# Kernel optimization log

Measured on AMD Instinct MI355X. Metric: run time of the kernel, lower is better.

Reference implementation:

```python
import math
import jax, jax.numpy as jnp
import numpy as np

EPS_LN = 1e-5
EPS_NORM = 1e-12


def conv2d(x, w, b=None, groups=1):
    # x: (B,C,H,W), w: (O, I//groups, kh, kw)
    out = jax.lax.conv_general_dilated(
        x, w, window_strides=(1, 1), padding='SAME',
        dimension_numbers=('NCHW', 'OIHW', 'NCHW'),
        feature_group_count=groups)
    if b is not None:
        out = out + b[None, :, None, None]
    return out


def layernorm2d(x, w, b):
    # LayerNorm over channel dim of (B,C,H,W)
    mu = x.mean(axis=1, keepdims=True)
    var = ((x - mu) ** 2).mean(axis=1, keepdims=True)
    xn = (x - mu) / jnp.sqrt(var + EPS_LN)
    return xn * w[None, :, None, None] + b[None, :, None, None]


def l2norm(x):
    n = jnp.sqrt((x * x).sum(axis=-1, keepdims=True))
    return x / jnp.maximum(n, EPS_NORM)


def mha(s, Wi, bi, Wo, bo, num_heads):
    # torch nn.MultiheadAttention (batch_first) self-attention
    B, S, C = s.shape
    Dh = C // num_heads
    qkv = s @ Wi.T + bi                      # (B,S,3C)
    q, k, v = jnp.split(qkv, 3, axis=-1)
    hd = lambda t: t.reshape(B, S, num_heads, Dh).transpose(0, 2, 1, 3)
    q, k, v = hd(q), hd(k), hd(v)            # (B,H,S,Dh)
    attn = jax.nn.softmax(jnp.einsum('bhqd,bhkd->bhqk', q, k) / math.sqrt(Dh), axis=-1)
    o = jnp.einsum('bhqk,bhkd->bhqd', attn, v).transpose(0, 2, 1, 3).reshape(B, S, C)
    return o @ Wo.T + bo


def frfn(x, pconv_w, lin1_w, lin1_b, dw_w, dw_b, lin2_w, lin2_b):
    b, c, h, w = x.shape
    dc = c // 4
    x1 = conv2d(x[:, :dc], pconv_w)                       # partial conv, no bias
    x = jnp.concatenate([x1, x[:, dc:]], axis=1)
    xt = x.transpose(0, 2, 3, 1).reshape(b, h * w, c)
    y = jax.nn.gelu(xt @ lin1_w.T + lin1_b, approximate=False)  # (b,hw,2*hid)
    y1, y2 = jnp.split(y, 2, axis=-1)
    hid = lin1_w.shape[0] // 2
    y1 = y1.reshape(b, h, w, hid).transpose(0, 3, 1, 2)
    y1 = jax.nn.gelu(conv2d(y1, dw_w, dw_b, groups=hid), approximate=False)
    y1 = y1.transpose(0, 2, 3, 1).reshape(b, h * w, hid)
    out = (y1 * y2) @ lin2_w.T + lin2_b
    return out.reshape(b, h, w, c).transpose(0, 3, 1, 2)


def setup_inputs() -> dict:
    key = jax.random.key(0)
    ks = jax.random.split(key, 10)
    B, C, H, W = 16, 256, 64, 64
    HID = 2 * C  # FRFN hidden = embed_dim*2
    DC = C // 4
    w = lambda k, shape: (jax.random.normal(k, shape, dtype=jnp.float32) * 0.02)
    return {
        'x': jax.random.normal(ks[0], (B, C, H, W), dtype=jnp.float32),
        'slot_scale': jnp.asarray(C ** -0.5, dtype=jnp.float32),
        'norm1_w': jnp.ones((C,), jnp.float32), 'norm1_b': jnp.zeros((C,), jnp.float32),
        'in_proj_w': w(ks[1], (3 * C, C)), 'in_proj_b': jnp.zeros((3 * C,), jnp.float32),
        'out_proj_w': w(ks[2], (C, C)), 'out_proj_b': jnp.zeros((C,), jnp.float32),
        'norm2_w': jnp.ones((C,), jnp.float32), 'norm2_b': jnp.zeros((C,), jnp.float32),
        'pconv_w': w(ks[3], (DC, DC, 3, 3)),
        'lin1_w': w(ks[4], (2 * HID, C)), 'lin1_b': jnp.zeros((2 * HID,), jnp.float32),
        'dw_w': w(ks[5], (HID, 1, 3, 3)), 'dw_b': jnp.zeros((HID,), jnp.float32),
        'lin2_w': w(ks[6], (C, HID)), 'lin2_b': jnp.zeros((C,), jnp.float32),
    }


def reference(x, slot_scale, norm1_w, norm1_b, in_proj_w, in_proj_b,
              out_proj_w, out_proj_b, norm2_w, norm2_b,
              pconv_w, lin1_w, lin1_b, dw_w, dw_b, lin2_w, lin2_b):
    NUM_HEADS, POOL = 8, 8
    b, c, h, w = x.shape
    copy = x
    # ada_avgpool slot init: 8x8 exact block means (h,w divisible by pool)
    pooled = x.reshape(b, c, POOL, h // POOL, POOL, w // POOL).mean(axis=(3, 5))  # (b,c,8,8)
    init_slots = pooled.transpose(0, 2, 3, 1).reshape(b, POOL * POOL, c)          # (b,S,c)

    shortcut = x
    xn = layernorm2d(x, norm1_w, norm1_b)
    xf = xn.transpose(0, 2, 3, 1).reshape(b, h * w, c)                            # (b,N,c)
    logits = slot_scale * jnp.einsum('bsc,bnc->bsn', l2norm(init_slots), l2norm(xf))
    slots = jnp.einsum('bsn,bnc->bsc', jax.nn.softmax(logits, axis=-1), xf)
    slots = mha(slots, in_proj_w, in_proj_b, out_proj_w, out_proj_b, NUM_HEADS)
    out = jnp.einsum('bns,bsc->bnc', jax.nn.softmax(logits.transpose(0, 2, 1), axis=-1), slots)
    out = out.transpose(0, 2, 1).reshape(b, c, h, w)

    x = shortcut + out
    x = x + frfn(layernorm2d(x, norm2_w, norm2_b),
                 pconv_w, lin1_w, lin1_b, dw_w, dw_b, lin2_w, lin2_b)
    return (x, copy - x)
```

## Files before the change

### kernel.cpp

```cpp
#include <hip/hip_runtime.h>
#include <hip/hip_bf16.h>
#include <stdint.h>
#include <math.h>

#define BB 16
#define CC 256
#define HH 64
#define WW 64
#define NN 4096
#define SS 64
#define NHEAD 8
#define DH 32
#define HID 512
#define DC 64

typedef float    f32x4  __attribute__((ext_vector_type(4)));
typedef uint16_t u16x8  __attribute__((ext_vector_type(8)));
typedef uint16_t u16x4  __attribute__((ext_vector_type(4)));
typedef uint16_t u16x2  __attribute__((ext_vector_type(2)));

__device__ __forceinline__ float gelu_fast(float x){
  float u = 0.7978845608028654f * (x + 0.044715f * x * x * x);
  float e = __expf(2.0f * u);
  float th = 1.0f - 2.0f / (e + 1.0f);
  return 0.5f * x * (1.0f + th);
}
__device__ __forceinline__ uint16_t f2b(float f){
  union { float f; uint32_t u; } v; v.f = f;
  uint32_t r = v.u + 0x7fffu + ((v.u >> 16) & 1u);
  return (uint16_t)(r >> 16);
}
__device__ __forceinline__ float b2f(uint16_t h){
  union { uint32_t u; float f; } v; v.u = ((uint32_t)h) << 16;
  return v.f;
}

__device__ __forceinline__ float waveSum(float v){
#pragma unroll
  for (int m = 32; m >= 1; m >>= 1) v += __shfl_xor(v, m, 64);
  return v;
}
__device__ __forceinline__ float blockSum256(float v, float* s4){
  v = waveSum(v);
  __syncthreads();
  if ((threadIdx.x & 63) == 0) s4[threadIdx.x >> 6] = v;
  __syncthreads();
  return s4[0] + s4[1] + s4[2] + s4[3];
}

__device__ __forceinline__ void g2l16(const void* g, void* l){
  __builtin_amdgcn_global_load_lds((const __attribute__((address_space(1))) uint32_t*)g,
                                   (__attribute__((address_space(3))) uint32_t*)l, 16, 0, 0);
}

__device__ __forceinline__ int swz8(int row, int kp){ return (kp ^ (row & 7)) << 3; }

__device__ __forceinline__ void mfma_bf16(f32x4& d, u16x8 a, u16x8 b){
  asm volatile("v_mfma_f32_16x16x32_bf16 %0, %1, %2, %0" : "+v"(d) : "v"(a), "v"(b));
}

template<int SWA, int SWB>
__device__ __forceinline__ void mma_core(const uint16_t* lA, int lda, const uint16_t* lB, int ldb,
                                         f32x4 (&acc)[4][4], int wrow, int wcol, int lane){
  const int rb = lane & 15, ub = lane >> 4;
#pragma unroll
  for (int ks = 0; ks < 2; ks++){
    const int u = ks * 4 + ub;
    u16x8 af[4], bf[4];
#pragma unroll
    for (int m = 0; m < 4; m++){
      int r = wrow + m * 16 + rb;
      int e = SWA ? ((u ^ (r & 7)) << 3) : (u << 3);
      af[m] = *(const u16x8*)&lA[r * lda + e];
    }
#pragma unroll
    for (int n = 0; n < 4; n++){
      int r = wcol + n * 16 + rb;
      int e = SWB ? ((u ^ (r & 7)) << 3) : (u << 3);
      bf[n] = *(const u16x8*)&lB[r * ldb + e];
    }
#pragma unroll
    for (int m = 0; m < 4; m++)
#pragma unroll
      for (int n = 0; n < 4; n++)
        mfma_bf16(acc[m][n], af[m], bf[n]);
  }
}

__global__ __launch_bounds__(256) void k_t2b(const float* __restrict__ in, uint16_t* __restrict__ out){
  __shared__ float tile[64][33];
  int b = blockIdx.z;
  int n0 = blockIdx.x * 32;
  int c0 = blockIdx.y * 64;
  int tx = threadIdx.x, ty = threadIdx.y;
  const float* src = in + (size_t)b * CC * NN;
#pragma unroll
  for (int i = 0; i < 64; i += 8)
    tile[ty + i][tx] = src[(size_t)(c0 + ty + i) * NN + n0 + tx];
  __syncthreads();
  uint16_t* dst = out + (size_t)b * NN * CC;
#pragma unroll
  for (int i = 0; i < 32; i += 8){
    int r = ty + i;
    u16x2 o; o[0] = f2b(tile[tx * 2][r]); o[1] = f2b(tile[tx * 2 + 1][r]);
    *(u16x2*)&dst[(size_t)(n0 + r) * CC + c0 + tx * 2] = o;
  }
}

__global__ __launch_bounds__(256) void k_pool(const uint16_t* __restrict__ xhwcb, uint16_t* __restrict__ slotsNb){
  int bs = blockIdx.x; int b = bs >> 6, s = bs & 63;
  int sy = (s >> 3) * 8, sx = (s & 7) * 8;
  int t = threadIdx.x;
  int c4 = t & 63, pg = t >> 6;
  const uint16_t* base = xhwcb + (size_t)b * NN * CC;
  float a0 = 0.f, a1 = 0.f, a2 = 0.f, a3 = 0.f;
#pragma unroll
  for (int i = 0; i < 16; i++){
    int p = pg * 16 + i; int py = p >> 3, px = p & 7;
    u16x4 v = *(const u16x4*)&base[(size_t)((sy + py) * WW + sx + px) * CC + c4 * 4];
    a0 += b2f(v[0]); a1 += b2f(v[1]); a2 += b2f(v[2]); a3 += b2f(v[3]);
  }
  __shared__ float sm[4][64][4];
  sm[pg][c4][0] = a0; sm[pg][c4][1] = a1; sm[pg][c4][2] = a2; sm[pg][c4][3] = a3;
  __syncthreads();
  if (t < 64){
    float v0 = (sm[0][t][0] + sm[1][t][0] + sm[2][t][0] + sm[3][t][0]) * (1.0f / 64.0f);
    float v1 = (sm[0][t][1] + sm[1][t][1] + sm[2][t][1] + sm[3][t][1]) * (1.0f / 64.0f);
    float v2 = (sm[0][t][2] + sm[1][t][2] + sm[2][t][2] + sm[3][t][2]) * (1.0f / 64.0f);
    float v3 = (sm[0][t][3] + sm[1][t][3] + sm[2][t][3] + sm[3][t][3]) * (1.0f / 64.0f);
    float ss = waveSum(v0 * v0 + v1 * v1 + v2 * v2 + v3 * v3);
    float inv = 1.0f / fmaxf(sqrtf(ss), 1e-12f);
    u16x4 o; o[0] = f2b(v0 * inv); o[1] = f2b(v1 * inv); o[2] = f2b(v2 * inv); o[3] = f2b(v3 * inv);
    *(u16x4*)&slotsNb[(size_t)bs * CC + t * 4] = o;
  }
}

__global__ __launch_bounds__(256) void k_ln_w(const uint16_t* __restrict__ xa, const uint16_t* __restrict__ xb,
                                              const float* __restrict__ w, const float* __restrict__ b,
                                              uint16_t* __restrict__ xoutb, float* __restrict__ rn,
                                              uint16_t* __restrict__ xn2p){
  int row = blockIdx.x * 4 + (threadIdx.x >> 6);
  int lane = threadIdx.x & 63;
  u16x4 va = *(const u16x4*)&xa[(size_t)row * CC + lane * 4];
  float v0 = b2f(va[0]), v1 = b2f(va[1]), v2 = b2f(va[2]), v3 = b2f(va[3]);
  if (xb){
    u16x4 vb = *(const u16x4*)&xb[(size_t)row * CC + lane * 4];
    v0 += b2f(vb[0]); v1 += b2f(vb[1]); v2 += b2f(vb[2]); v3 += b2f(vb[3]);
  }
  float mu = waveSum(v0 + v1 + v2 + v3) * (1.0f / CC);
  float d0 = v0 - mu, d1 = v1 - mu, d2 = v2 - mu, d3 = v3 - mu;
  float var = waveSum(d0 * d0 + d1 * d1 + d2 * d2 + d3 * d3) * (1.0f / CC);
  float inv = rsqrtf(var + 1e-5f);
  float4 wv = *(const float4*)&w[lane * 4];
  float4 bv = *(const float4*)&b[lane * 4];
  float x0 = d0 * inv * wv.x + bv.x;
  float x1 = d1 * inv * wv.y + bv.y;
  float x2 = d2 * inv * wv.z + bv.z;
  float x3 = d3 * inv * wv.w + bv.w;
  u16x4 o; o[0] = f2b(x0); o[1] = f2b(x1); o[2] = f2b(x2); o[3] = f2b(x3);
  *(u16x4*)&xoutb[(size_t)row * CC + lane * 4] = o;
  if (xn2p && lane < 16){
    int bb = row >> 12, n = row & 4095, y = n >> 6, x = n & 63;
    *(u16x4*)&xn2p[(((size_t)(bb * 66 + y + 1)) * 66 + x + 1) * 64 + lane * 4] = o;
  }
  if (rn){
    float ss = waveSum(x0 * x0 + x1 * x1 + x2 * x2 + x3 * x3);
    if (lane == 0) rn[row] = 1.0f / fmaxf(sqrtf(ss), 1e-12f);
  }
}

__global__ __launch_bounds__(256) void k_zb(uint16_t* __restrict__ xn2p){
  int i = blockIdx.x * 256 + threadIdx.x;
  if (i >= 16 * 260 * 16) return;
  int c4 = i & 15; int rest = i >> 4;
  int j = rest % 260; int b = rest / 260;
  int py, px;
  if (j < 66){ py = 0; px = j; }
  else if (j < 132){ py = 65; px = j - 66; }
  else if (j < 196){ py = j - 132 + 1; px = 0; }
  else { py = j - 196 + 1; px = 65; }
  u16x4 z; z[0] = 0; z[1] = 0; z[2] = 0; z[3] = 0;
  *(u16x4*)&xn2p[(((size_t)(b * 66 + py)) * 66 + px) * 64 + c4 * 4] = z;
}

__global__ __launch_bounds__(256) void k_cvtw(const float* __restrict__ wi, const float* __restrict__ wo,
                                              const float* __restrict__ w1, const float* __restrict__ w2,
                                              const float* __restrict__ pw, const float* __restrict__ dww,
                                              uint16_t* __restrict__ wib, uint16_t* __restrict__ wob,
                                              uint16_t* __restrict__ w1b, uint16_t* __restrict__ w2b,
                                              uint16_t* __restrict__ wp2, float* __restrict__ dwwT){
  int i = blockIdx.x * 256 + threadIdx.x;
  if (i < 163840){
    const float* src; uint16_t* dst; int off;
    if (i < 49152){ src = wi; dst = wib; off = i; }
    else if (i < 65536){ src = wo; dst = wob; off = i - 49152; }
    else if (i < 131072){ src = w1; dst = w1b; off = i - 65536; }
    else { src = w2; dst = w2b; off = i - 131072; }
    float4 v = ((const float4*)src)[off];
    u16x4 o;
    o[0] = f2b(v.x); o[1] = f2b(v.y); o[2] = f2b(v.z); o[3] = f2b(v.w);
    *(u16x4*)&dst[(size_t)off * 4] = o;
  } else if (i < 200704){
    int j = i - 163840;
    if (j < 64 * 576){
      int co = j / 576, r = j % 576, tap = r >> 6, ci = r & 63;
      wp2[j] = f2b(pw[(size_t)co * 576 + ci * 9 + tap]);
    }
  } else {
    int j = i - 200704;
    if (j < 9 * HID){
      int tap = j / HID, ch = j % HID;
      dwwT[j] = dww[(size_t)ch * 9 + tap];
    }
  }
}

__global__ __launch_bounds__(256) void k_logits_mfma(const uint16_t* __restrict__ slotsNb,
                                                     const uint16_t* __restrict__ xnb,
                                                     const float* __restrict__ rn,
                                                     const float* __restrict__ scale_p,
                                                     uint16_t* __restrict__ E){
  __shared__ uint16_t smem[20480];
  __shared__ float rnS[256];
  uint16_t* lA = smem;
  uint16_t* lB = smem + 64 * 64;
  int t = threadIdx.x, lane = t & 63, w = t >> 6;
  int b = blockIdx.y, n0 = blockIdx.x * 256;
  rnS[t] = rn[b * NN + n0 + t];
  f32x4 acc[4][4];
#pragma unroll
  for (int m = 0; m < 4; m++)
#pragma unroll
    for (int n = 0; n < 4; n++) acc[m][n] = (f32x4){0.f, 0.f, 0.f, 0.f};
  for (int kc = 0; kc < 4; kc++){
#pragma unroll
    for (int i = 0; i < 2; i++){
      int idx = i * 256 + t, row = idx >> 3, kp = idx & 7;
      *(u16x8*)&lA[row * 64 + swz8(row, kp)] = *(const u16x8*)&slotsNb[(size_t)(b * 64 + row) * 256 + kc * 64 + kp * 8];
    }
#pragma unroll
    for (int i = 0; i < 8; i++){
      int idx = i * 256 + t, row = idx >> 3, kp = idx & 7;
      *(u16x8*)&lB[row * 64 + swz8(row, kp)] = *(const u16x8*)&xnb[((size_t)b * NN + n0 + row) * 256 + kc * 64 + kp * 8];
    }
    __syncthreads();
    mma_core<1, 1>(lA, 64, lB, 64, acc, 0, w * 64, lane);
    __syncthreads();
  }
  float scale = scale_p[0];
  int rb4 = (lane >> 4) * 4, cb = lane & 15;
#pragma unroll
  for (int m = 0; m < 4; m++)
#pragma unroll
    for (int n = 0; n < 4; n++)
#pragma unroll
      for (int j = 0; j < 4; j++){
        int s = m * 16 + rb4 + j, nl = w * 64 + n * 16 + cb;
        smem[s * 264 + nl] = f2b(__expf(acc[m][n][j] * scale * rnS[nl]));
      }
  __syncthreads();
#pragma unroll
  for (int i = 0; i < 8; i++){
    int idx = i * 256 + t, row = idx >> 5, cseg = idx & 31;
    *(u16x8*)&E[((size_t)b * 64 + row) * NN + n0 + cseg * 8] = *(const u16x8*)&smem[row * 264 + cseg * 8];
  }
}

__global__ __launch_bounds__(256) void k_z1(const uint16_t* __restrict__ E, float* __restrict__ invz1){
  int bs = blockIdx.x, t = threadIdx.x;
  u16x8 v0 = *(const u16x8*)&E[(size_t)bs * NN + t * 16];
  u16x8 v1 = *(const u16x8*)&E[(size_t)bs * NN + t * 16 + 8];
  float s = 0.f;
#pragma unroll
  for (int i = 0; i < 8; i++) s += b2f(v0[i]) + b2f(v1[i]);
  __shared__ float s4[4];
  float z = blockSum256(s, s4);
  if (t == 0) invz1[bs] = 1.0f / z;
}

__global__ __launch_bounds__(256) void k_slots_mfma(const uint16_t* __restrict__ E,
                                                    const uint16_t* __restrict__ xnb,
                                                    float* __restrict__ part){
  __shared__ uint16_t lA[64 * 64];
  __shared__ uint16_t lB[256 * 72];
  int t = threadIdx.x, lane = t & 63, w = t >> 6;
  int ks = blockIdx.x, b = blockIdx.y;
  f32x4 acc[4][4];
#pragma unroll
  for (int m = 0; m < 4; m++)
#pragma unroll
    for (int n = 0; n < 4; n++) acc[m][n] = (f32x4){0.f, 0.f, 0.f, 0.f};
  for (int kc = 0; kc < 8; kc++){
    int n0 = ks * 512 + kc * 64;
#pragma unroll
    for (int i = 0; i < 2; i++){
      int idx = i * 256 + t, row = idx >> 3, kp = idx & 7;
      *(u16x8*)&lA[row * 64 + swz8(row, kp)] = *(const u16x8*)&E[((size_t)b * 64 + row) * NN + n0 + kp * 8];
    }
#pragma unroll
    for (int i = 0; i < 8; i++){
      int idx = i * 256 + t, nrow = idx >> 5, cseg = idx & 31;
      u16x8 v = *(const u16x8*)&xnb[((size_t)b * NN + n0 + nrow) * 256 + cseg * 8];
#pragma unroll
      for (int j = 0; j < 8; j++) lB[(cseg * 8 + j) * 72 + nrow] = v[j];
    }
    __syncthreads();
    mma_core<1, 0>(lA, 64, lB, 72, acc, 0, w * 64, lane);
    __syncthreads();
  }
  int rb4 = (lane >> 4) * 4, cb = lane & 15;
#pragma unroll
  for (int m = 0; m < 4; m++)
#pragma unroll
    for (int n = 0; n < 4; n++)
#pragma unroll
      for (int j = 0; j < 4; j++){
        int s = m * 16 + rb4 + j, c = w * 64 + n * 16 + cb;
        part[(((size_t)b * 8 + ks) * 64 + s) * 256 + c] = acc[m][n][j];
      }
}

__global__ __launch_bounds__(256) void k_fold(const float* __restrict__ part, const float* __restrict__ invz1,
                                              uint16_t* __restrict__ slotsb){
  int i = blockIdx.x * 256 + threadIdx.x;
  int row = i >> 6, c4 = i & 63;
  int b = row >> 6, s = row & 63;
  float4 a = {0.f, 0.f, 0.f, 0.f};
#pragma unroll
  for (int p = 0; p < 8; p++){
    float4 v = *(const float4*)&part[(((size_t)b * 8 + p) * 64 + s) * 256 + c4 * 4];
    a.x += v.x; a.y += v.y; a.z += v.z; a.w += v.w;
  }
  float iz = invz1[row];
  u16x4 o; o[0] = f2b(a.x * iz); o[1] = f2b(a.y * iz); o[2] = f2b(a.z * iz); o[3] = f2b(a.w * iz);
  *(u16x4*)&slotsb[(size_t)row * 256 + c4 * 4] = o;
}

__global__ __launch_bounds__(256) void k_gemm_qkv(const uint16_t* __restrict__ slotsb,
                                                  const uint16_t* __restrict__ wib,
                                                  const float* __restrict__ bi,
                                                  float* __restrict__ qkv){
  __shared__ uint16_t lA[128 * 64];
  __shared__ uint16_t lB[128 * 64];
  int t = threadIdx.x, lane = t & 63, w = t >> 6;
  int wrow = (w >> 1) * 64, wcol = (w & 1) * 64;
  int BR = blockIdx.x * 128, BC = blockIdx.y * 128;
  f32x4 acc[4][4];
#pragma unroll
  for (int m = 0; m < 4; m++)
#pragma unroll
    for (int n = 0; n < 4; n++) acc[m][n] = (f32x4){0.f, 0.f, 0.f, 0.f};
  for (int kc = 0; kc < 4; kc++){
#pragma unroll
    for (int i = 0; i < 4; i++){
      int idx = i * 256 + t, row = idx >> 3, kp = idx & 7;
      *(u16x8*)&lA[row * 64 + swz8(row, kp)] = *(const u16x8*)&slotsb[(size_t)(BR + row) * 256 + kc * 64 + kp * 8];
      *(u16x8*)&lB[row * 64 + swz8(row, kp)] = *(const u16x8*)&wib[(size_t)(BC + row) * 256 + kc * 64 + kp * 8];
    }
    __syncthreads();
    mma_core<1, 1>(lA, 64, lB, 64, acc, wrow, wcol, lane);
    __syncthreads();
  }
  int rb4 = (lane >> 4) * 4, cb = lane & 15;
#pragma unroll
  for (int m = 0; m < 4; m++)
#pragma unroll
    for (int n = 0; n < 4; n++){
      int c = BC + wcol + n * 16 + cb;
      float bias = bi[c];
#pragma unroll
      for (int j = 0; j < 4; j++)
        qkv[(size_t)(BR + wrow + m * 16 + rb4 + j) * 768 + c] = acc[m][n][j] + bias;
    }
}

__global__ __launch_bounds__(256) void k_attn(const float* __restrict__ qkv, uint16_t* __restrict__ aob){
  int b = blockIdx.x >> 3, h = blockIdx.x & 7;
  __shared__ float lq[64][33], lk[64][33], lv[64][33];
  __shared__ float sc[64][65];
  int t = threadIdx.x;
  for (int idx = t; idx < 64 * 32; idx += 256){
    int s = idx >> 5, d = idx & 31;
    const float* base = qkv + ((size_t)b * SS + s) * 768 + h * DH + d;
    lq[s][d] = base[0];
    lk[s][d] = base[256];
    lv[s][d] = base[512];
  }
  __syncthreads();
  const float rs = 0.17677669529663687f;
  for (int idx = t; idx < 64 * 64; idx += 256){
    int qq = idx >> 6, kk = idx & 63;
    float a = 0.f;
#pragma unroll
    for (int d = 0; d < 32; d++) a += lq[qq][d] * lk[kk][d];
    sc[qq][kk] = a * rs;
  }
  __syncthreads();
  {
    int r = t >> 2, sub = t & 3;
    float m = -1e30f;
#pragma unroll
    for (int k = sub * 16; k < sub * 16 + 16; k++) m = fmaxf(m, sc[r][k]);
    m = fmaxf(m, __shfl_xor(m, 1, 64));
    m = fmaxf(m, __shfl_xor(m, 2, 64));
    float z = 0.f;
#pragma unroll
    for (int k = sub * 16; k < sub * 16 + 16; k++){
      float e = __expf(sc[r][k] - m); sc[r][k] = e; z += e;
    }
    z += __shfl_xor(z, 1, 64);
    z += __shfl_xor(z, 2, 64);
    float iv = 1.0f / z;
#pragma unroll
    for (int k = sub * 16; k < sub * 16 + 16; k++) sc[r][k] *= iv;
  }
  __syncthreads();
  for (int idx = t; idx < 64 * 32; idx += 256){
    int qq = idx >> 5, d = idx & 31;
    float a = 0.f;
#pragma unroll
    for (int k = 0; k < 64; k++) a += sc[qq][k] * lv[k][d];
    aob[((size_t)b * SS + qq) * CC + h * DH + d] = f2b(a);
  }
}

__global__ __launch_bounds__(256) void k_gemm_oproj(const uint16_t* __restrict__ aob,
                                                    const uint16_t* __restrict__ wob,
                                                    const float* __restrict__ bo,
                                                    uint16_t* __restrict__ sl2Tb){
  __shared__ uint16_t lA[128 * 64];
  __shared__ uint16_t lB[128 * 64];
  int t = threadIdx.x, lane = t & 63, w = t >> 6;
  int wrow = (w >> 1) * 64, wcol = (w & 1) * 64;
  int BR = blockIdx.x * 128, BC = blockIdx.y * 128;
  f32x4 acc[4][4];
#pragma unroll
  for (int m = 0; m < 4; m++)
#pragma unroll
    for (int n = 0; n < 4; n++) acc[m][n] = (f32x4){0.f, 0.f, 0.f, 0.f};
  for (int kc = 0; kc < 4; kc++){
#pragma unroll
    for (int i = 0; i < 4; i++){
      int idx = i * 256 + t, row = idx >> 3, kp = idx & 7;
      *(u16x8*)&lA[row * 64 + swz8(row, kp)] = *(const u16x8*)&aob[(size_t)(BR + row) * 256 + kc * 64 + kp * 8];
      *(u16x8*)&lB[row * 64 + swz8(row, kp)] = *(const u16x8*)&wob[(size_t)(BC + row) * 256 + kc * 64 + kp * 8];
    }
    __syncthreads();
    mma_core<1, 1>(lA, 64, lB, 64, acc, wrow, wcol, lane);
    __syncthreads();
  }
  int rb4 = (lane >> 4) * 4, cb = lane & 15;
#pragma unroll
  for (int m = 0; m < 4; m++)
#pragma unroll
    for (int n = 0; n < 4; n++){
      int c = BC + wcol + n * 16 + cb;
      float bias = bo[c];
#pragma unroll
      for (int j = 0; j < 4; j++){
        int r = BR + wrow + m * 16 + rb4 + j;
        int b = r >> 6, s = r & 63;
        sl2Tb[((size_t)b * 256 + c) * 64 + s] = f2b(acc[m][n][j] + bias);
      }
    }
}

__global__ __launch_bounds__(256) void k_mix(const uint16_t* __restrict__ E, const uint16_t* __restrict__ sl2Tb,
                                             uint16_t* __restrict__ mixb){
  __shared__ uint16_t lA[128 * 72];
  __shared__ uint16_t lB[128 * 64];
  __shared__ float z2S[128];
  int t = threadIdx.x, lane = t & 63, w = t >> 6;
  int wrow = (w >> 1) * 64, wcol = (w & 1) * 64;
  int BR = blockIdx.x * 128, BC = blockIdx.y * 128, b = blockIdx.z;
#pragma unroll
  for (int i = 0; i < 4; i++){
    int idx = i * 256 + t; int s = idx >> 4, n8 = (idx & 15) * 8;
    u16x8 v = *(const u16x8*)&E[((size_t)b * 64 + s) * NN + BR + n8];
#pragma unroll
    for (int j = 0; j < 8; j++) lA[(n8 + j) * 72 + s] = v[j];
  }
#pragma unroll
  for (int i = 0; i < 4; i++){
    int idx = i * 256 + t, row = idx >> 3, kp = idx & 7;
    *(u16x8*)&lB[row * 64 + swz8(row, kp)] = *(const u16x8*)&sl2Tb[((size_t)b * 256 + BC + row) * 64 + kp * 8];
  }
  __syncthreads();
  if (t < 128){
    float s = 0.f;
#pragma unroll
    for (int k2 = 0; k2 < 64; k2++) s += b2f(lA[t * 72 + k2]);
    z2S[t] = 1.0f / s;
  }
  __syncthreads();
  f32x4 acc[4][4];
#pragma unroll
  for (int m = 0; m < 4; m++)
#pragma unroll
    for (int n = 0; n < 4; n++) acc[m][n] = (f32x4){0.f, 0.f, 0.f, 0.f};
  mma_core<0, 1>(lA, 72, lB, 64, acc, wrow, wcol, lane);
  int rb4 = (lane >> 4) * 4, cb = lane & 15;
#pragma unroll
  for (int m = 0; m < 4; m++)
#pragma unroll
    for (int n = 0; n < 4; n++)
#pragma unroll
      for (int j = 0; j < 4; j++){
        int lrow = wrow + m * 16 + rb4 + j;
        size_t gi = ((size_t)b * NN + BR + lrow) * 256 + BC + wcol + n * 16 + cb;
        mixb[gi] = f2b(acc[m][n][j] * z2S[lrow]);
      }
}

__global__ __launch_bounds__(256) void k_pconv_mfma(const uint16_t* __restrict__ xn2p,
                                                    const uint16_t* __restrict__ wp2,
                                                    uint16_t* __restrict__ pcb){
  __shared__ uint16_t lA[256 * 64];
  __shared__ uint16_t lB[64 * 64];
  int t = threadIdx.x, lane = t & 63, w = t >> 6;
  int wrow = w * 64;
  int BR = blockIdx.x * 256;
  f32x4 acc[4][4];
#pragma unroll
  for (int m = 0; m < 4; m++)
#pragma unroll
    for (int n = 0; n < 4; n++) acc[m][n] = (f32x4){0.f, 0.f, 0.f, 0.f};
  for (int tap = 0; tap < 9; tap++){
    int dy = tap / 3 - 1, dx = tap % 3 - 1;
#pragma unroll
    for (int i = 0; i < 8; i++){
      int q = (w * 8 + i) * 64 + lane;
      int row = q >> 3, kpe = swz8(row, q & 7);
      int r = BR + row;
      int b = r >> 12, n = r & 4095, y = n >> 6, x = n & 63;
      size_t p = ((size_t)(b * 66 + (y + 1 + dy)) * 66 + (x + 1 + dx)) * 64 + kpe;
      g2l16(&xn2p[p], &lA[(w * 8 + i) * 512]);
    }
#pragma unroll
    for (int i = 0; i < 2; i++){
      int q = (w * 2 + i) * 64 + lane;
      int row = q >> 3, kpe = swz8(row, q & 7);
      g2l16(&wp2[(size_t)row * 576 + tap * 64 + kpe], &lB[(w * 2 + i) * 512]);
    }
    __syncthreads();
    mma_core<1, 1>(lA, 64, lB, 64, acc, wrow, 0, lane);
    __syncthreads();
  }
  int rb4 = (lane >> 4) * 4, cb = lane & 15;
#pragma unroll
  for (int m = 0; m < 4; m++)
#pragma unroll
    for (int n = 0; n < 4; n++)
#pragma unroll
      for (int j = 0; j < 4; j++)
        pcb[(size_t)(BR + wrow + m * 16 + rb4 + j) * 64 + (n * 16 + cb)] = f2b(acc[m][n][j]);
}

__global__ __launch_bounds__(256) void k_lin1_mfma(const uint16_t* __restrict__ pcb,
                                                   const uint16_t* __restrict__ xn2b,
                                                   const uint16_t* __restrict__ w1b,
                                                   const float* __restrict__ b1,
                                                   uint16_t* __restrict__ Y1b, uint16_t* __restrict__ Y2b){
  __shared__ uint16_t lA[128 * 64];
  __shared__ uint16_t lB[128 * 64];
  int t = threadIdx.x, lane = t & 63, w = t >> 6;
  int wrow = (w >> 1) * 64, wcol = (w & 1) * 64;
  int bid = blockIdx.x;
  int xcd = bid & 7, i5 = bid >> 3;
  int BR = (xcd * 64 + (i5 >> 3)) * 128;
  int BC = (i5 & 7) * 128;
  f32x4 acc[4][4];
#pragma unroll
  for (int m = 0; m < 4; m++)
#pragma unroll
    for (int n = 0; n < 4; n++) acc[m][n] = (f32x4){0.f, 0.f, 0.f, 0.f};
  for (int kc = 0; kc < 4; kc++){
#pragma unroll
    for (int i = 0; i < 4; i++){
      int q = (w * 4 + i) * 64 + lane;
      int row = q >> 3, kpe = swz8(row, q & 7);
      size_t gr = (size_t)(BR + row);
      const uint16_t* src = (kc == 0) ? &pcb[gr * 64 + kpe] : &xn2b[gr * 256 + kc * 64 + kpe];
      g2l16(src, &lA[(w * 4 + i) * 512]);
      g2l16(&w1b[(size_t)(BC + row) * 256 + kc * 64 + kpe], &lB[(w * 4 + i) * 512]);
    }
    __syncthreads();
    mma_core<1, 1>(lA, 64, lB, 64, acc, wrow, wcol, lane);
    __syncthreads();
  }
  int rb4 = (lane >> 4) * 4, cb = lane & 15;
#pragma unroll
  for (int m = 0; m < 4; m++){
#pragma unroll
    for (int n = 0; n < 4; n++){
      int c = BC + wcol + n * 16 + cb;
      float bias = b1[c];
#pragma unroll
      for (int j = 0; j < 4; j++){
        size_t r = (size_t)(BR + wrow + m * 16 + rb4 + j);
        uint16_t h = f2b(gelu_fast(acc[m][n][j] + bias));
        if (c < HID) Y1b[r * HID + c] = h;
        else         Y2b[r * HID + (c - HID)] = h;
      }
    }
  }
}

__global__ __launch_bounds__(256) void k_dwconv(const uint16_t* __restrict__ Y1b,
                                                const float* __restrict__ dwwT,
                                                const float* __restrict__ dwb,
                                                const uint16_t* __restrict__ Y2b,
                                                uint16_t* __restrict__ YPb){
  __shared__ uint16_t lds[3 * 18 * 136];
  int b = blockIdx.z, chunk = blockIdx.y;
  int y = blockIdx.x >> 2, seg = blockIdx.x & 3;
  int x0 = seg * 16;
  int t = threadIdx.x;
  const uint16_t* base = Y1b + (size_t)b * NN * HID + chunk * 128;
  const u16x8 z = {0, 0, 0, 0, 0, 0, 0, 0};
#pragma unroll
  for (int i = 0; i < 4; i++){
    int idx = i * 256 + t;
    if (idx < 864){
      int g8 = idx & 15, rest = idx >> 4;
      int c = rest % 18, r = rest / 18;
      int ry = y + r - 1, xx = x0 + c - 1;
      u16x8 v = z;
      if (ry >= 0 && ry < HH && xx >= 0 && xx < WW)
        v = *(const u16x8*)&base[(size_t)(ry * WW + xx) * HID + g8 * 8];
      *(u16x8*)&lds[(r * 18 + c) * 136 + g8 * 8] = v;
    }
  }
  __syncthreads();
  int px = t >> 4, g8 = t & 15;
  int cg = chunk * 128 + g8 * 8;
  int n = y * WW + x0 + px;
  u16x8 y2 = *(const u16x8*)&Y2b[((size_t)b * NN + n) * HID + cg];
  float acc[8];
  {
    float4 b0 = *(const float4*)&dwb[cg];
    float4 b1 = *(const float4*)&dwb[cg + 4];
    acc[0] = b0.x; acc[1] = b0.y; acc[2] = b0.z; acc[3] = b0.w;
    acc[4] = b1.x; acc[5] = b1.y; acc[6] = b1.z; acc[7] = b1.w;
  }
#pragma unroll
  for (int r = 0; r < 3; r++)
#pragma unroll
    for (int dx = 0; dx < 3; dx++){
      u16x8 v = *(const u16x8*)&lds[(r * 18 + px + dx) * 136 + g8 * 8];
      const float* wt = &dwwT[(r * 3 + dx) * HID + cg];
      float4 w0 = *(const float4*)wt;
      float4 w1 = *(const float4*)(wt + 4);
      acc[0] += b2f(v[0]) * w0.x; acc[1] += b2f(v[1]) * w0.y;
      acc[2] += b2f(v[2]) * w0.z; acc[3] += b2f(v[3]) * w0.w;
      acc[4] += b2f(v[4]) * w1.x; acc[5] += b2f(v[5]) * w1.y;
      acc[6] += b2f(v[6]) * w1.z; acc[7] += b2f(v[7]) * w1.w;
    }
  u16x8 o;
#pragma unroll
  for (int j = 0; j < 8; j++) o[j] = f2b(gelu_fast(acc[j]) * b2f(y2[j]));
  *(u16x8*)&YPb[((size_t)b * NN + n) * HID + cg] = o;
}

__global__ __launch_bounds__(256) void k_lin2_mfma(const uint16_t* __restrict__ YPb,
                                                   const uint16_t* __restrict__ w2b,
                                                   const float* __restrict__ b2,
                                                   uint16_t* __restrict__ deltab){
  __shared__ uint16_t lA[128 * 64];
  __shared__ uint16_t lB[128 * 64];
  int t = threadIdx.x, lane = t & 63, w = t >> 6;
  int wrow = (w >> 1) * 64, wcol = (w & 1) * 64;
  int bid = blockIdx.x;
  int xcd = bid & 7, i5 = bid >> 3;
  int BR = (xcd * 64 + (i5 >> 1)) * 128;
  int BC = (i5 & 1) * 128;
  f32x4 acc[4][4];
#pragma unroll
  for (int m = 0; m < 4; m++)
#pragma unroll
    for (int n = 0; n < 4; n++) acc[m][n] = (f32x4){0.f, 0.f, 0.f, 0.f};
  for (int kc = 0; kc < 8; kc++){
#pragma unroll
    for (int i = 0; i < 4; i++){
      int q = (w * 4 + i) * 64 + lane;
      int row = q >> 3, kpe = swz8(row, q & 7);
      g2l16(&YPb[(size_t)(BR + row) * HID + kc * 64 + kpe], &lA[(w * 4 + i) * 512]);
      g2l16(&w2b[(size_t)(BC + row) * HID + kc * 64 + kpe], &lB[(w * 4 + i) * 512]);
    }
    __syncthreads();
    mma_core<1, 1>(lA, 64, lB, 64, acc, wrow, wcol, lane);
    __syncthreads();
  }
  int rb4 = (lane >> 4) * 4, cb = lane & 15;
#pragma unroll
  for (int m = 0; m < 4; m++){
#pragma unroll
    for (int n = 0; n < 4; n++){
      int c = BC + wcol + n * 16 + cb;
      float bias = b2[c];
#pragma unroll
      for (int j = 0; j < 4; j++){
        size_t gr = (size_t)(BR + wrow + m * 16 + rb4 + j);
        deltab[gr * CC + c] = f2b(acc[m][n][j] + bias);
      }
    }
  }
}

__global__ __launch_bounds__(256) void k_final2(const uint16_t* __restrict__ mixb,
                                                const uint16_t* __restrict__ deltab,
                                                const uint16_t* __restrict__ xhwcb,
                                                float* __restrict__ out){
  __shared__ float t0[64 * 68];
  __shared__ float t1[64 * 68];
  int b = blockIdx.z;
  int n0 = blockIdx.x * 64, c0 = blockIdx.y * 64;
  int t = threadIdx.x;
#pragma unroll
  for (int i = 0; i < 4; i++){
    int idx = i * 256 + t, row = idx >> 4, c4 = idx & 15;
    size_t gp = ((size_t)b * NN + n0 + row) * CC + c0 + c4 * 4;
    u16x4 m = *(const u16x4*)&mixb[gp];
    u16x4 d = *(const u16x4*)&deltab[gp];
    u16x4 xh = *(const u16x4*)&xhwcb[gp];
    f32x4 v0, v1;
#pragma unroll
    for (int j = 0; j < 4; j++){
      float v = b2f(m[j]) + b2f(d[j]);
      v0[j] = b2f(xh[j]) + v;
      v1[j] = -v;
    }
    *(f32x4*)&t0[row * 68 + c4 * 4] = v0;
    *(f32x4*)&t1[row * 68 + c4 * 4] = v1;
  }
  __syncthreads();
  int cl = t >> 2, seg = t & 3;
  float* o1 = out + (size_t)BB * CC * NN;
  size_t gbase = ((size_t)(b * CC + c0 + cl)) * NN + n0 + seg * 16;
#pragma unroll
  for (int k = 0; k < 4; k++){
    float4 a, c;
    a.x = t0[(seg * 16 + k * 4 + 0) * 68 + cl];
    a.y = t0[(seg * 16 + k * 4 + 1) * 68 + cl];
    a.z = t0[(seg * 16 + k * 4 + 2) * 68 + cl];
    a.w = t0[(seg * 16 + k * 4 + 3) * 68 + cl];
    c.x = t1[(seg * 16 + k * 4 + 0) * 68 + cl];
    c.y = t1[(seg * 16 + k * 4 + 1) * 68 + cl];
    c.z = t1[(seg * 16 + k * 4 + 2) * 68 + cl];
    c.w = t1[(seg * 16 + k * 4 + 3) * 68 + cl];
    *(float4*)&out[gbase + k * 4] = a;
    *(float4*)&o1[gbase + k * 4] = c;
  }
}

extern "C" void kernel_launch(void* const* d_in, const int* in_sizes, int n_in,
                              void* d_out, int out_size, void* d_ws, size_t ws_size,
                              hipStream_t stream){
  const float* x       = (const float*)d_in[0];
  const float* scale_p = (const float*)d_in[1];
  const float* n1w     = (const float*)d_in[2];
  const float* n1b     = (const float*)d_in[3];
  const float* wi      = (const float*)d_in[4];
  const float* bi      = (const float*)d_in[5];
  const float* wo      = (const float*)d_in[6];
  const float* bo      = (const float*)d_in[7];
  const float* n2w     = (const float*)d_in[8];
  const float* n2b     = (const float*)d_in[9];
  const float* pw      = (const float*)d_in[10];
  const float* w1      = (const float*)d_in[11];
  const float* b1      = (const float*)d_in[12];
  const float* dww     = (const float*)d_in[13];
  const float* dwb     = (const float*)d_in[14];
  const float* w2      = (const float*)d_in[15];
  const float* b2      = (const float*)d_in[16];

  float* base = (float*)d_ws;
  size_t off = 0;
  float* part = base + off; off += (size_t)BB * 8 * SS * CC;
  float* QKV  = base + off; off += (size_t)BB * SS * 3 * CC;
  float* RN   = base + off; off += (size_t)BB * NN;
  float* IZ1  = base + off; off += (size_t)BB * SS;
  float* dwwT = base + off; off += (size_t)9 * HID;
  uint16_t* slotsNb = (uint16_t*)(base + off); off += (size_t)BB * SS * CC / 2;
  uint16_t* slotsb  = (uint16_t*)(base + off); off += (size_t)BB * SS * CC / 2;
  uint16_t* aob     = (uint16_t*)(base + off); off += (size_t)BB * SS * CC / 2;
  uint16_t* sl2Tb   = (uint16_t*)(base + off); off += (size_t)BB * CC * SS / 2;
  uint16_t* xhwcb   = (uint16_t*)(base + off); off += (size_t)BB * NN * CC / 2;
  uint16_t* xnb     = (uint16_t*)(base + off); off += (size_t)BB * NN * CC / 2;
  uint16_t* mixb    = (uint16_t*)(base + off); off += (size_t)BB * NN * CC / 2;
  uint16_t* deltab  = (uint16_t*)(base + off); off += (size_t)BB * NN * CC / 2;
  uint16_t* E       = (uint16_t*)(base + off); off += (size_t)BB * SS * NN / 2;
  uint16_t* w1b     = (uint16_t*)(base + off); off += (size_t)(2 * HID) * CC / 2;
  uint16_t* w2b     = (uint16_t*)(base + off); off += (size_t)CC * HID / 2;
  uint16_t* wib     = (uint16_t*)(base + off); off += (size_t)(3 * CC) * CC / 2;
  uint16_t* wob     = (uint16_t*)(base + off); off += (size_t)CC * CC / 2;
  uint16_t* wp2     = (uint16_t*)(base + off); off += (size_t)64 * 576 / 2 + 16;
  uint16_t* Y1b     = (uint16_t*)(base + off); off += (size_t)BB * NN * HID / 2;
  uint16_t* Y2b     = (uint16_t*)(base + off); off += (size_t)BB * NN * HID / 2;
  uint16_t* YPb     = (uint16_t*)(base + off); off += (size_t)BB * NN * HID / 2;
  uint16_t* xn2b    = (uint16_t*)(base + off); off += (size_t)BB * NN * CC / 2;
  uint16_t* xn2p    = (uint16_t*)(base + off); off += (size_t)BB * 66 * 66 * 64 / 2;
  uint16_t* pcb     = (uint16_t*)(base + off); off += (size_t)BB * NN * 64 / 2;
  if (ws_size < off * sizeof(float)) return;
  float* OUT = (float*)d_out;

  dim3 tb2(32, 8);
  k_t2b<<<dim3(NN / 32, CC / 64, BB), tb2, 0, stream>>>(x, xhwcb);
  k_pool<<<BB * SS, 256, 0, stream>>>(xhwcb, slotsNb);
  k_ln_w<<<BB * NN / 4, 256, 0, stream>>>(xhwcb, (const uint16_t*)nullptr, n1w, n1b, xnb, RN,
                                          (uint16_t*)nullptr);
  k_cvtw<<<803, 256, 0, stream>>>(wi, wo, w1, w2, pw, dww, wib, wob, w1b, w2b, wp2, dwwT);
  k_zb<<<(16 * 260 * 16 + 255) / 256, 256, 0, stream>>>(xn2p);
  k_logits_mfma<<<dim3(NN / 256, BB), 256, 0, stream>>>(slotsNb, xnb, RN, scale_p, E);
  k_z1<<<BB * SS, 256, 0, stream>>>(E, IZ1);
  k_slots_mfma<<<dim3(8, BB), 256, 0, stream>>>(E, xnb, part);
  k_fold<<<(BB * SS * CC / 4) / 256, 256, 0, stream>>>(part, IZ1, slotsb);
  k_gemm_qkv<<<dim3(8, 6), 256, 0, stream>>>(slotsb, wib, bi, QKV);
  k_attn<<<BB * NHEAD, 256, 0, stream>>>(QKV, aob);
  k_gemm_oproj<<<dim3(8, 2), 256, 0, stream>>>(aob, wob, bo, sl2Tb);
  k_mix<<<dim3(NN / 128, CC / 128, BB), 256, 0, stream>>>(E, sl2Tb, mixb);
  k_ln_w<<<BB * NN / 4, 256, 0, stream>>>(xhwcb, mixb, n2w, n2b, xn2b, (float*)nullptr, xn2p);
  k_pconv_mfma<<<BB * NN / 256, 256, 0, stream>>>(xn2p, wp2, pcb);
  k_lin1_mfma<<<4096, 256, 0, stream>>>(pcb, xn2b, w1b, b1, Y1b, Y2b);
  k_dwconv<<<dim3(256, 4, BB), 256, 0, stream>>>(Y1b, dwwT, dwb, Y2b, YPb);
  k_lin2_mfma<<<1024, 256, 0, stream>>>(YPb, w2b, b2, deltab);
  k_final2<<<dim3(NN / 64, CC / 64, BB), 256, 0, stream>>>(mixb, deltab, xhwcb, OUT);
}
```

Before: 464.0 us.

## Pre-transpose normalized activations so slots GEMM loads B via direct LDS copies

Adds a transpose kernel that writes the layer-normed activations in channel-major order (b,c,n). The slots GEMM then loads both operands with swizzled direct global-to-LDS 16-byte copies instead of scattering 8 scalar LDS stores per vector for an in-kernel transpose. This is meant to cut LDS bank traffic and the VGPR round trip in the slots kernel, which runs on only 128 blocks. In exchange it adds an extra full pass that reads and writes a 32 MB bf16 tensor, plus an additional workspace buffer.

```diff
diff --git a/kernel.cpp b/kernel.cpp
--- a/kernel.cpp
+++ b/kernel.cpp
@@ -215,6 +215,26 @@
   }
 }
 
+__global__ __launch_bounds__(256) void k_txT(const uint16_t* __restrict__ xnb, uint16_t* __restrict__ xnTb){
+  __shared__ uint16_t tile[64 * 66];
+  int b = blockIdx.z;
+  int n0 = blockIdx.x * 64, c0 = blockIdx.y * 64;
+  int t = threadIdx.x;
+#pragma unroll
+  for (int i = 0; i < 16; i++){
+    int idx = i * 256 + t;
+    int nr = idx >> 6, c = idx & 63;
+    tile[c * 66 + nr] = xnb[((size_t)b * NN + n0 + nr) * CC + c0 + c];
+  }
+  __syncthreads();
+#pragma unroll
+  for (int i = 0; i < 16; i++){
+    int idx = i * 256 + t;
+    int cr = idx >> 6, n = idx & 63;
+    xnTb[((size_t)b * CC + c0 + cr) * NN + n0 + n] = tile[cr * 66 + n];
+  }
+}
+
 __global__ __launch_bounds__(256) void k_logits_mfma(const uint16_t* __restrict__ slotsNb,
                                                      const uint16_t* __restrict__ xnb,
                                                      const float* __restrict__ rn,
@@ -279,10 +299,10 @@
 }
 
 __global__ __launch_bounds__(256) void k_slots_mfma(const uint16_t* __restrict__ E,
-                                                    const uint16_t* __restrict__ xnb,
+                                                    const uint16_t* __restrict__ xnTb,
                                                     float* __restrict__ part){
   __shared__ uint16_t lA[64 * 64];
-  __shared__ uint16_t lB[256 * 72];
+  __shared__ uint16_t lB[256 * 64];
   int t = threadIdx.x, lane = t & 63, w = t >> 6;
   int ks = blockIdx.x, b = blockIdx.y;
   f32x4 acc[4][4];
@@ -294,18 +314,18 @@
     int n0 = ks * 512 + kc * 64;
 #pragma unroll
     for (int i = 0; i < 2; i++){
-      int idx = i * 256 + t, row = idx >> 3, kp = idx & 7;
-      *(u16x8*)&lA[row * 64 + swz8(row, kp)] = *(const u16x8*)&E[((size_t)b * 64 + row) * NN + n0 + kp * 8];
+      int q = (w * 2 + i) * 64 + lane;
+      int row = q >> 3, kpe = swz8(row, q & 7);
+      g2l16(&E[((size_t)b * 64 + row) * NN + n0 + kpe], &lA[(w * 2 + i) * 512]);
     }
 #pragma unroll
     for (int i = 0; i < 8; i++){
-      int idx = i * 256 + t, nrow = idx >> 5, cseg = idx & 31;
-      u16x8 v = *(const u16x8*)&xnb[((size_t)b * NN + n0 + nrow) * 256 + cseg * 8];
-#pragma unroll
-      for (int j = 0; j < 8; j++) lB[(cseg * 8 + j) * 72 + nrow] = v[j];
-    }
-    __syncthreads();
-    mma_core<1, 0>(lA, 64, lB, 72, acc, 0, w * 64, lane);
+      int q = (w * 8 + i) * 64 + lane;
+      int row = q >> 3, kpe = swz8(row, q & 7);
+      g2l16(&xnTb[((size_t)b * CC + row) * NN + n0 + kpe], &lB[(w * 8 + i) * 512]);
+    }
+    __syncthreads();
+    mma_core<1, 1>(lA, 64, lB, 64, acc, 0, w * 64, lane);
     __syncthreads();
   }
   int rb4 = (lane >> 4) * 4, cb = lane & 15;
@@ -787,6 +807,7 @@
   uint16_t* sl2Tb   = (uint16_t*)(base + off); off += (size_t)BB * CC * SS / 2;
   uint16_t* xhwcb   = (uint16_t*)(base + off); off += (size_t)BB * NN * CC / 2;
   uint16_t* xnb     = (uint16_t*)(base + off); off += (size_t)BB * NN * CC / 2;
+  uint16_t* xnTb    = (uint16_t*)(base + off); off += (size_t)BB * NN * CC / 2;
   uint16_t* mixb    = (uint16_t*)(base + off); off += (size_t)BB * NN * CC / 2;
   uint16_t* deltab  = (uint16_t*)(base + off); off += (size_t)BB * NN * CC / 2;
   uint16_t* E       = (uint16_t*)(base + off); off += (size_t)BB * SS * NN / 2;
@@ -812,8 +833,9 @@
   k_cvtw<<<803, 256, 0, stream>>>(wi, wo, w1, w2, pw, dww, wib, wob, w1b, w2b, wp2, dwwT);
   k_zb<<<(16 * 260 * 16 + 255) / 256, 256, 0, stream>>>(xn2p);
   k_logits_mfma<<<dim3(NN / 256, BB), 256, 0, stream>>>(slotsNb, xnb, RN, scale_p, E);
+  k_txT<<<dim3(NN / 64, CC / 64, BB), 256, 0, stream>>>(xnb, xnTb);
   k_z1<<<BB * SS, 256, 0, stream>>>(E, IZ1);
-  k_slots_mfma<<<dim3(8, BB), 256, 0, stream>>>(E, xnb, part);
+  k_slots_mfma<<<dim3(8, BB), 256, 0, stream>>>(E, xnTb, part);
   k_fold<<<(BB * SS * CC / 4) / 256, 256, 0, stream>>>(part, IZ1, slotsb);
   k_gemm_qkv<<<dim3(8, 6), 256, 0, stream>>>(slotsb, wib, bi, QKV);
   k_attn<<<BB * NHEAD, 256, 0, stream>>>(QKV, aob);
```

After: 428.9 us. -7.6%, faster.
